# Optimization experiments

Hardware: AMD Instinct MI355X
Metric: run time of the kernel (lower is better)

Reference implementation:

```python
import jax, jax.numpy as jnp
import numpy as np

# Model dims (from module defaults / chosen plant dims)
B, T = 1024, 1024
NY, NX, NW, NU = 32, 16, 128, 8   # input(obs), state, nonlin, output(action)
DT = 0.01
N_ITER_COLD = 30   # torchdeq f_max_iter
N_ITER_WARM = 5    # solver_kwargs f_max_iter when reusing warm start
LOG_STD_INIT = -1.6094379124341003


def setup_inputs() -> dict:
    key = jax.random.key(0)
    ks = jax.random.split(key, 11)
    s = 0.1  # keep the implicit/recurrent dynamics stable over 1024 RK4 steps
    obs = jax.random.normal(ks[0], (B, T, NY), jnp.float32)
    x0 = jnp.zeros((B, NX), jnp.float32)
    A_T = (-0.5 * jnp.eye(NX) + 0.05 * jax.random.normal(ks[1], (NX, NX))).astype(jnp.float32)
    Bw_T = s * jax.random.normal(ks[2], (NW, NX), jnp.float32)
    By_T = s * jax.random.normal(ks[3], (NY, NX), jnp.float32)
    Cv_T = s * jax.random.normal(ks[4], (NX, NW), jnp.float32)
    Dvw_T = 0.05 * jax.random.normal(ks[5], (NW, NW), jnp.float32)  # small -> fixed-point contraction
    Dvy_T = s * jax.random.normal(ks[6], (NY, NW), jnp.float32)
    Cu_T = s * jax.random.normal(ks[7], (NX, NU), jnp.float32)
    Duw_T = s * jax.random.normal(ks[8], (NW, NU), jnp.float32)
    Duy_T = s * jax.random.normal(ks[9], (NY, NU), jnp.float32)
    log_stds = LOG_STD_INIT * jnp.ones((NU,), jnp.float32)
    return dict(obs=obs, x0=x0, A_T=A_T, Bw_T=Bw_T, By_T=By_T, Cv_T=Cv_T,
                Dvw_T=Dvw_T, Dvy_T=Dvy_T, Cu_T=Cu_T, Duw_T=Duw_T, Duy_T=Duy_T,
                log_stds=log_stds)


def reference(obs, x0, A_T, Bw_T, By_T, Cv_T, Dvw_T, Dvy_T, Cu_T, Duw_T, Duy_T, log_stds):
    def fp_solve(w0, bias, n_iter):
        # w = tanh(x@Cv_T + w@Dvw_T + y@Dvy_T); bias = x@Cv_T + y@Dvy_T precomputed
        def body(i, w):
            return jnp.tanh(bias + w @ Dvw_T)
        return jax.lax.fori_loop(0, n_iter, body, w0)

    def xdot(x, w, y):
        return x @ A_T + w @ Bw_T + y @ By_T

    def step(x, y, w_guess, n_w):
        y_bias = y @ Dvy_T  # [B, NW], reused across RK stages
        wk = fp_solve(w_guess, x @ Cv_T + y_bias, n_w)
        k1 = xdot(x, wk, y)
        def stage(xs, w_prev):
            ws = fp_solve(w_prev, xs @ Cv_T + y_bias, N_ITER_WARM)
            return xdot(xs, ws, y), ws
        k2, w2 = stage(x + 0.5 * DT * k1, wk)
        k3, w3 = stage(x + 0.5 * DT * k2, w2)
        k4, w4 = stage(x + DT * k3, w3)
        x_next = x + (DT / 6.0) * (k1 + 2.0 * k2 + 2.0 * k3 + k4)
        u = x @ Cu_T + wk @ Duw_T + y @ Duy_T  # action from current state/nonlin/obs
        return x_next, w4, u

    # First timestep: cold DEQ solve (30 iters), no warm start
    w0 = jnp.zeros((x0.shape[0], NW), x0.dtype)
    x1, wg, u0 = step(x0, obs[:, 0], w0, N_ITER_COLD)

    # Remaining timesteps: warm-started solves (5 iters), sequential via scan
    def scan_body(carry, y_t):
        x, wg = carry
        x_next, w_next, u = step(x, y_t, wg, N_ITER_WARM)
        return (x_next, w_next), u
    obs_rest = jnp.swapaxes(obs[:, 1:], 0, 1)  # [T-1, B, NY]
    _, us = jax.lax.scan(scan_body, (x1, wg), obs_rest)

    actions = jnp.concatenate([u0[:, None, :], jnp.swapaxes(us, 0, 1)], axis=1)  # [B, T, NU]
    outputs = jnp.concatenate(
        [actions, jnp.broadcast_to(log_stds, actions.shape)], axis=-1)  # [B, T, 2*NU]
    return outputs
```

## Files before the change

### kernel.cpp

```cpp
#include <hip/hip_runtime.h>
#include <hip/hip_bf16.h>


#define T_SZ 1024
#define NY 32
#define NX 16
#define NW 128
#define NU 8
#define DT_F 0.01f
#define NCOLD 30
#define NWARM 5
#define KAPPA 2.8853900817779268f

typedef __attribute__((ext_vector_type(8))) short bf8v;
typedef __attribute__((ext_vector_type(4))) float f4v;

#define MFMA16(a, b, c) __builtin_amdgcn_mfma_f32_16x16x32_bf16((a), (b), (c), 0, 0, 0)

__device__ __forceinline__ unsigned short f2bf(float f) {
  return __builtin_bit_cast(unsigned short, __float2bfloat16(f));
}
__device__ __forceinline__ float bf2f(unsigned short u) {
  return __bfloat162float(__builtin_bit_cast(__hip_bfloat16, u));
}
__device__ __forceinline__ short tanh_bf(float z) {
  float e = __builtin_amdgcn_exp2f(z);
  float r = __builtin_amdgcn_rcpf(e + 1.0f);
  return (short)f2bf(1.0f - 2.0f * r);
}

__global__ __launch_bounds__(256, 1) void rinn_kernel(
    const float* __restrict__ obs, const float* __restrict__ x0,
    const float* __restrict__ A_T, const float* __restrict__ Bw_T,
    const float* __restrict__ By_T, const float* __restrict__ Cv_T,
    const float* __restrict__ Dvw_T, const float* __restrict__ Dvy_T,
    const float* __restrict__ Cu_T, const float* __restrict__ Duw_T,
    const float* __restrict__ Duy_T, const float* __restrict__ log_stds,
    float* __restrict__ out) {
  __shared__ __align__(16) char wlds[8192];
  __shared__ __align__(16) char xlds[4096];

  const int tid = (int)threadIdx.x;
  const int wv = tid >> 6;
  const int lane = tid & 63;
  const int r = lane & 15;
  const int h = lane >> 4;
  const long grow = (long)(blockIdx.x * 16 + r);
  const int sw = (r & 7) << 4;
  const int rbase = r * 256;

  const int ro0 = (64 * wv + 16 * h) ^ sw;
  const int ro1 = (64 * ((wv + 1) & 3) + 16 * h) ^ sw;
  const int ro2 = (64 * ((wv + 2) & 3) + 16 * h) ^ sw;
  const int ro3 = (64 * ((wv + 3) & 3) + 16 * h) ^ sw;

  bf8v Adw[2][4], Acv[2], Ady[2];
#pragma unroll
  for (int gi = 0; gi < 2; ++gi) {
    const int j = 32 * wv + 8 * (r >> 2) + 4 * gi + (r & 3);
#pragma unroll
    for (int s = 0; s < 4; ++s) {
      const int f = (wv + s) & 3;
#pragma unroll
      for (int q = 0; q < 8; ++q)
        Adw[gi][s][q] = (short)f2bf(KAPPA * Dvw_T[(32 * f + 8 * h + q) * NW + j]);
    }
#pragma unroll
    for (int q = 0; q < 8; ++q) {
      Acv[gi][q] = (short)f2bf(KAPPA * Cv_T[((8 * h + q) & 15) * NW + j]);
      Ady[gi][q] = (short)f2bf(KAPPA * Dvy_T[(8 * h + q) * NW + j]);
    }
  }
  bf8v Ax, Akx[4], Ayx, Au, Aku[4], Ayu;
#pragma unroll
  for (int q = 0; q < 8; ++q) {
    int k = 8 * h + q;
    Ax[q] = (short)f2bf(A_T[(k & 15) * NX + r]);
    Ayx[q] = (short)f2bf(By_T[k * NX + r]);
    float cu = 0.f, dy = 0.f;
    if (wv == 1 && r < NU) { cu = Cu_T[(k & 15) * NU + r]; dy = Duy_T[k * NU + r]; }
    Au[q] = (short)f2bf(cu);
    Ayu[q] = (short)f2bf(dy);
  }
#pragma unroll
  for (int s = 0; s < 4; ++s) {
    const int f = (wv + s) & 3;
#pragma unroll
    for (int q = 0; q < 8; ++q) {
      int k = 32 * f + 8 * h + q;
      Akx[s][q] = (short)f2bf(Bw_T[k * NX + r]);
      float du = 0.f;
      if (wv == 1 && r < NU) du = Duw_T[k * NU + r];
      Aku[s][q] = (short)f2bf(du);
    }
  }
  f4v lsv;
#pragma unroll
  for (int i = 0; i < 4; ++i) lsv[i] = (h >= 2) ? log_stds[4 * (h - 2) + i] : 0.f;

  f4v xr;
#pragma unroll
  for (int i = 0; i < 4; ++i) xr[i] = x0[grow * NX + 4 * h + i];

  char* xbase = xlds + wv * 1024;
  auto write_x = [&](f4v v) {
    unsigned short b0 = f2bf(v[0]), b1 = f2bf(v[1]), b2 = f2bf(v[2]), b3 = f2bf(v[3]);
    uint2 hp, lp;
    hp.x = (unsigned)b0 | ((unsigned)b1 << 16);
    hp.y = (unsigned)b2 | ((unsigned)b3 << 16);
    lp.x = (unsigned)f2bf(v[0] - bf2f(b0)) | ((unsigned)f2bf(v[1] - bf2f(b1)) << 16);
    lp.y = (unsigned)f2bf(v[2] - bf2f(b2)) | ((unsigned)f2bf(v[3] - bf2f(b3)) << 16);
    *(uint2*)(xbase + r * 64 + 8 * h) = hp;
    *(uint2*)(xbase + r * 64 + 32 + 8 * h) = lp;
  };
  auto read_bx = [&]() { return *(const bf8v*)(xbase + r * 64 + 16 * h); };

  {
    uint4 z; z.x = z.y = z.z = z.w = 0u;
    ((uint4*)wlds)[tid] = z;
    write_x(xr);
  }
  __syncthreads();

  const float* orow = obs + grow * T_SZ * NY;
  bf8v By0, By1;
  {
    float yf[8];
#pragma unroll
    for (int q = 0; q < 8; ++q) yf[q] = orow[8 * h + q];
#pragma unroll
    for (int q = 0; q < 8; ++q) {
      unsigned short hi = f2bf(yf[q]);
      By0[q] = (short)hi;
      By1[q] = (short)f2bf(yf[q] - bf2f(hi));
    }
  }

  int co = 0;
  bf8v of8 = {};
  f4v cbias0, cbias1;

  auto solve_iter = [&]() {
    const char* wb = wlds + co;
    bf8v b1 = *(const bf8v*)(wb + rbase + ro1);
    bf8v b2 = *(const bf8v*)(wb + rbase + ro2);
    bf8v b3 = *(const bf8v*)(wb + rbase + ro3);
    f4v c0 = MFMA16(Adw[0][0], of8, cbias0);
    f4v c1 = MFMA16(Adw[1][0], of8, cbias1);
    c0 = MFMA16(Adw[0][1], b1, c0);  c1 = MFMA16(Adw[1][1], b1, c1);
    c0 = MFMA16(Adw[0][2], b2, c0);  c1 = MFMA16(Adw[1][2], b2, c1);
    c0 = MFMA16(Adw[0][3], b3, c0);  c1 = MFMA16(Adw[1][3], b3, c1);
    bf8v o;
    o[0] = tanh_bf(c0[0]); o[1] = tanh_bf(c0[1]); o[2] = tanh_bf(c0[2]); o[3] = tanh_bf(c0[3]);
    o[4] = tanh_bf(c1[0]); o[5] = tanh_bf(c1[1]); o[6] = tanh_bf(c1[2]); o[7] = tanh_bf(c1[3]);
    of8 = o;
    *(bf8v*)(wlds + (co ^ 4096) + rbase + ro0) = o;
    __syncthreads();
    co ^= 4096;
  };

  auto kchain = [&](bf8v bx, int t, bool do_u) -> f4v {
    const char* wb = wlds + co;
    bf8v b1 = *(const bf8v*)(wb + rbase + ro1);
    bf8v b2 = *(const bf8v*)(wb + rbase + ro2);
    bf8v b3 = *(const bf8v*)(wb + rbase + ro3);
    f4v z = {0.f, 0.f, 0.f, 0.f};
    f4v c = MFMA16(Ax, bx, z);
    c = MFMA16(Akx[0], of8, c);
    c = MFMA16(Akx[1], b1, c); c = MFMA16(Akx[2], b2, c); c = MFMA16(Akx[3], b3, c);
    c = MFMA16(Ayx, By0, c);   c = MFMA16(Ayx, By1, c);
    if (do_u && wv == 1) {
      f4v cu = MFMA16(Au, bx, z);
      cu = MFMA16(Aku[0], of8, cu);
      cu = MFMA16(Aku[1], b1, cu); cu = MFMA16(Aku[2], b2, cu); cu = MFMA16(Aku[3], b3, cu);
      cu = MFMA16(Ayu, By0, cu);   cu = MFMA16(Ayu, By1, cu);
      f4v sv;
#pragma unroll
      for (int i = 0; i < 4; ++i) sv[i] = (h < 2) ? cu[i] : lsv[i];
      *(f4v*)(out + (grow * T_SZ + t) * 16 + 4 * h) = sv;
    }
    return c;
  };

  for (int t = 0; t < T_SZ; ++t) {
    f4v zz = {0.f, 0.f, 0.f, 0.f};
    f4v cb0 = MFMA16(Ady[0], By0, zz); cb0 = MFMA16(Ady[0], By1, cb0);
    f4v cb1 = MFMA16(Ady[1], By0, zz); cb1 = MFMA16(Ady[1], By1, cb1);

    bf8v bx = read_bx();
    cbias0 = MFMA16(Acv[0], bx, cb0); cbias1 = MFMA16(Acv[1], bx, cb1);
    const int n1 = (t == 0) ? NCOLD : NWARM;
    for (int it = 0; it < n1; ++it) solve_iter();
    float yn[8];
    {
      const long tn = (t + 1 < T_SZ) ? (t + 1) : t;
#pragma unroll
      for (int q = 0; q < 8; ++q) yn[q] = orow[tn * NY + 8 * h + q];
    }
    f4v kv = kchain(bx, t, true);
    f4v acc = kv, xs;
#pragma unroll
    for (int i = 0; i < 4; ++i) xs[i] = xr[i] + (0.5f * DT_F) * kv[i];
    write_x(xs);

    bx = read_bx();
    cbias0 = MFMA16(Acv[0], bx, cb0); cbias1 = MFMA16(Acv[1], bx, cb1);
    for (int it = 0; it < NWARM; ++it) solve_iter();
    kv = kchain(bx, t, false);
#pragma unroll
    for (int i = 0; i < 4; ++i) { acc[i] += 2.f * kv[i]; xs[i] = xr[i] + (0.5f * DT_F) * kv[i]; }
    write_x(xs);

    bx = read_bx();
    cbias0 = MFMA16(Acv[0], bx, cb0); cbias1 = MFMA16(Acv[1], bx, cb1);
    for (int it = 0; it < NWARM; ++it) solve_iter();
    kv = kchain(bx, t, false);
#pragma unroll
    for (int i = 0; i < 4; ++i) { acc[i] += 2.f * kv[i]; xs[i] = xr[i] + DT_F * kv[i]; }
    write_x(xs);

    bx = read_bx();
    cbias0 = MFMA16(Acv[0], bx, cb0); cbias1 = MFMA16(Acv[1], bx, cb1);
    for (int it = 0; it < NWARM; ++it) solve_iter();
    kv = kchain(bx, t, false);
#pragma unroll
    for (int i = 0; i < 4; ++i) xr[i] += (DT_F / 6.f) * (acc[i] + kv[i]);
    write_x(xr);

#pragma unroll
    for (int q = 0; q < 8; ++q) {
      unsigned short hi = f2bf(yn[q]);
      By0[q] = (short)hi;
      By1[q] = (short)f2bf(yn[q] - bf2f(hi));
    }
  }
}

extern "C" void kernel_launch(void* const* d_in, const int* in_sizes, int n_in,
                              void* d_out, int out_size, void* d_ws, size_t ws_size,
                              hipStream_t stream) {
  (void)in_sizes; (void)n_in; (void)out_size; (void)d_ws; (void)ws_size;
  rinn_kernel<<<64, 256, 0, stream>>>(
      (const float*)d_in[0], (const float*)d_in[1], (const float*)d_in[2],
      (const float*)d_in[3], (const float*)d_in[4], (const float*)d_in[5],
      (const float*)d_in[6], (const float*)d_in[7], (const float*)d_in[8],
      (const float*)d_in[9], (const float*)d_in[10], (const float*)d_in[11],
      (float*)d_out);
}
```

Measured before the change: 6.200 ms.

## Fuse k-chain with next stage's first solve iteration and shuffle x via bpermute

Each RK stage's xdot computation is merged with the first fixed-point iteration of the following stage, so both share one set of LDS reads of w and one barrier. The x state is no longer passed through LDS; it is moved into MFMA fragment layout with ds_bpermute. __syncthreads is replaced by a custom barrier that waits only on LDS counters, which removes the per-stage barriers and LDS round-trips. The restructured loop must reproduce the original iteration counts, and the lighter barrier relies on only LDS traffic needing ordering.

```diff
diff --git a/kernel.cpp b/kernel.cpp
--- a/kernel.cpp
+++ b/kernel.cpp
@@ -28,6 +28,11 @@
   float r = __builtin_amdgcn_rcpf(e + 1.0f);
   return (short)f2bf(1.0f - 2.0f * r);
 }
+__device__ __forceinline__ void wave_barrier() {
+  asm volatile("s_waitcnt lgkmcnt(0)" ::: "memory");
+  __builtin_amdgcn_s_barrier();
+  asm volatile("" ::: "memory");
+}
 
 __global__ __launch_bounds__(256, 1) void rinn_kernel(
     const float* __restrict__ obs, const float* __restrict__ x0,
@@ -38,7 +43,6 @@
     const float* __restrict__ Duy_T, const float* __restrict__ log_stds,
     float* __restrict__ out) {
   __shared__ __align__(16) char wlds[8192];
-  __shared__ __align__(16) char xlds[4096];
 
   const int tid = (int)threadIdx.x;
   const int wv = tid >> 6;
@@ -54,6 +58,10 @@
   const int ro2 = (64 * ((wv + 2) & 3) + 16 * h) ^ sw;
   const int ro3 = (64 * ((wv + 3) & 3) + 16 * h) ^ sw;
 
+  const int ti0 = 4 * (r + 16 * ((2 * h) & 3));
+  const int ti1 = 4 * (r + 16 * ((2 * h + 1) & 3));
+  const bool hi_sel = (h < 2);
+
   bf8v Adw[2][4], Acv[2], Ady[2];
 #pragma unroll
   for (int gi = 0; gi < 2; ++gi) {
@@ -102,25 +110,10 @@
 #pragma unroll
   for (int i = 0; i < 4; ++i) xr[i] = x0[grow * NX + 4 * h + i];
 
-  char* xbase = xlds + wv * 1024;
-  auto write_x = [&](f4v v) {
-    unsigned short b0 = f2bf(v[0]), b1 = f2bf(v[1]), b2 = f2bf(v[2]), b3 = f2bf(v[3]);
-    uint2 hp, lp;
-    hp.x = (unsigned)b0 | ((unsigned)b1 << 16);
-    hp.y = (unsigned)b2 | ((unsigned)b3 << 16);
-    lp.x = (unsigned)f2bf(v[0] - bf2f(b0)) | ((unsigned)f2bf(v[1] - bf2f(b1)) << 16);
-    lp.y = (unsigned)f2bf(v[2] - bf2f(b2)) | ((unsigned)f2bf(v[3] - bf2f(b3)) << 16);
-    *(uint2*)(xbase + r * 64 + 8 * h) = hp;
-    *(uint2*)(xbase + r * 64 + 32 + 8 * h) = lp;
-  };
-  auto read_bx = [&]() { return *(const bf8v*)(xbase + r * 64 + 16 * h); };
-
   {
     uint4 z; z.x = z.y = z.z = z.w = 0u;
     ((uint4*)wlds)[tid] = z;
-    write_x(xr);
-  }
-  __syncthreads();
+  }
 
   const float* orow = obs + grow * T_SZ * NY;
   bf8v By0, By1;
@@ -135,10 +128,43 @@
       By1[q] = (short)f2bf(yf[q] - bf2f(hi));
     }
   }
+  wave_barrier();
+
+  auto x_to_bfrag = [&](f4v v) -> bf8v {
+    unsigned short hb0 = f2bf(v[0]), hb1 = f2bf(v[1]), hb2 = f2bf(v[2]), hb3 = f2bf(v[3]);
+    unsigned hiP0 = (unsigned)hb0 | ((unsigned)hb1 << 16);
+    unsigned hiP1 = (unsigned)hb2 | ((unsigned)hb3 << 16);
+    unsigned loP0 = (unsigned)f2bf(v[0] - bf2f(hb0)) | ((unsigned)f2bf(v[1] - bf2f(hb1)) << 16);
+    unsigned loP1 = (unsigned)f2bf(v[2] - bf2f(hb2)) | ((unsigned)f2bf(v[3] - bf2f(hb3)) << 16);
+    int a0 = __builtin_amdgcn_ds_bpermute(ti0, (int)hiP0);
+    int a1 = __builtin_amdgcn_ds_bpermute(ti0, (int)hiP1);
+    int a2 = __builtin_amdgcn_ds_bpermute(ti1, (int)hiP0);
+    int a3 = __builtin_amdgcn_ds_bpermute(ti1, (int)hiP1);
+    int b0 = __builtin_amdgcn_ds_bpermute(ti0, (int)loP0);
+    int b1_ = __builtin_amdgcn_ds_bpermute(ti0, (int)loP1);
+    int b2_ = __builtin_amdgcn_ds_bpermute(ti1, (int)loP0);
+    int b3_ = __builtin_amdgcn_ds_bpermute(ti1, (int)loP1);
+    int4 d;
+    d.x = hi_sel ? a0 : b0;
+    d.y = hi_sel ? a1 : b1_;
+    d.z = hi_sel ? a2 : b2_;
+    d.w = hi_sel ? a3 : b3_;
+    return __builtin_bit_cast(bf8v, d);
+  };
+
+  f4v cb0, cb1, cbias0, cbias1, acc;
+  bf8v bxc;
+  {
+    f4v z4 = {0.f, 0.f, 0.f, 0.f};
+    cb0 = MFMA16(Ady[0], By0, z4); cb0 = MFMA16(Ady[0], By1, cb0);
+    cb1 = MFMA16(Ady[1], By0, z4); cb1 = MFMA16(Ady[1], By1, cb1);
+    bxc = x_to_bfrag(xr);
+    cbias0 = MFMA16(Acv[0], bxc, cb0);
+    cbias1 = MFMA16(Acv[1], bxc, cb1);
+  }
 
   int co = 0;
   bf8v of8 = {};
-  f4v cbias0, cbias1;
 
   auto solve_iter = [&]() {
     const char* wb = wlds + co;
@@ -155,84 +181,94 @@
     o[4] = tanh_bf(c1[0]); o[5] = tanh_bf(c1[1]); o[6] = tanh_bf(c1[2]); o[7] = tanh_bf(c1[3]);
     of8 = o;
     *(bf8v*)(wlds + (co ^ 4096) + rbase + ro0) = o;
-    __syncthreads();
+    wave_barrier();
     co ^= 4096;
   };
 
-  auto kchain = [&](bf8v bx, int t, bool do_u) -> f4v {
+  for (int it = 0; it < NCOLD - 4; ++it) solve_iter();
+
+  float yn[8];
+
+  auto fusedB = [&](int mode, int t) {
     const char* wb = wlds + co;
     bf8v b1 = *(const bf8v*)(wb + rbase + ro1);
     bf8v b2 = *(const bf8v*)(wb + rbase + ro2);
     bf8v b3 = *(const bf8v*)(wb + rbase + ro3);
-    f4v z = {0.f, 0.f, 0.f, 0.f};
-    f4v c = MFMA16(Ax, bx, z);
-    c = MFMA16(Akx[0], of8, c);
-    c = MFMA16(Akx[1], b1, c); c = MFMA16(Akx[2], b2, c); c = MFMA16(Akx[3], b3, c);
-    c = MFMA16(Ayx, By0, c);   c = MFMA16(Ayx, By1, c);
-    if (do_u && wv == 1) {
-      f4v cu = MFMA16(Au, bx, z);
+    f4v z4 = {0.f, 0.f, 0.f, 0.f};
+    f4v kv = MFMA16(Ax, bxc, z4);
+    kv = MFMA16(Akx[0], of8, kv);
+    kv = MFMA16(Ayx, By0, kv);  kv = MFMA16(Ayx, By1, kv);
+    kv = MFMA16(Akx[1], b1, kv); kv = MFMA16(Akx[2], b2, kv); kv = MFMA16(Akx[3], b3, kv);
+    if (mode == 1 && wv == 1) {
+      f4v cu = MFMA16(Au, bxc, z4);
       cu = MFMA16(Aku[0], of8, cu);
+      cu = MFMA16(Ayu, By0, cu);  cu = MFMA16(Ayu, By1, cu);
       cu = MFMA16(Aku[1], b1, cu); cu = MFMA16(Aku[2], b2, cu); cu = MFMA16(Aku[3], b3, cu);
-      cu = MFMA16(Ayu, By0, cu);   cu = MFMA16(Ayu, By1, cu);
       f4v sv;
 #pragma unroll
       for (int i = 0; i < 4; ++i) sv[i] = (h < 2) ? cu[i] : lsv[i];
       *(f4v*)(out + (grow * T_SZ + t) * 16 + 4 * h) = sv;
     }
-    return c;
+    f4v xs;
+    if (mode == 1) {
+      acc = kv;
+#pragma unroll
+      for (int i = 0; i < 4; ++i) xs[i] = xr[i] + (0.5f * DT_F) * kv[i];
+    } else if (mode == 2) {
+#pragma unroll
+      for (int i = 0; i < 4; ++i) { acc[i] += 2.f * kv[i]; xs[i] = xr[i] + (0.5f * DT_F) * kv[i]; }
+    } else if (mode == 3) {
+#pragma unroll
+      for (int i = 0; i < 4; ++i) { acc[i] += 2.f * kv[i]; xs[i] = xr[i] + DT_F * kv[i]; }
+    } else {
+#pragma unroll
+      for (int i = 0; i < 4; ++i) xr[i] += (DT_F / 6.f) * (acc[i] + kv[i]);
+      xs = xr;
+    }
+    bf8v bxn = x_to_bfrag(xs);
+    if (mode == 4) {
+#pragma unroll
+      for (int q = 0; q < 8; ++q) {
+        unsigned short hi = f2bf(yn[q]);
+        By0[q] = (short)hi;
+        By1[q] = (short)f2bf(yn[q] - bf2f(hi));
+      }
+      cb0 = MFMA16(Ady[0], By0, z4); cb0 = MFMA16(Ady[0], By1, cb0);
+      cb1 = MFMA16(Ady[1], By0, z4); cb1 = MFMA16(Ady[1], By1, cb1);
+    }
+    cbias0 = MFMA16(Acv[0], bxn, cb0);
+    cbias1 = MFMA16(Acv[1], bxn, cb1);
+    f4v d0 = MFMA16(Adw[0][0], of8, z4);
+    d0 = MFMA16(Adw[0][1], b1, d0); d0 = MFMA16(Adw[0][2], b2, d0); d0 = MFMA16(Adw[0][3], b3, d0);
+    f4v d1 = MFMA16(Adw[1][0], of8, z4);
+    d1 = MFMA16(Adw[1][1], b1, d1); d1 = MFMA16(Adw[1][2], b2, d1); d1 = MFMA16(Adw[1][3], b3, d1);
+    f4v c0, c1;
+#pragma unroll
+    for (int i = 0; i < 4; ++i) { c0[i] = d0[i] + cbias0[i]; c1[i] = d1[i] + cbias1[i]; }
+    bf8v o;
+    o[0] = tanh_bf(c0[0]); o[1] = tanh_bf(c0[1]); o[2] = tanh_bf(c0[2]); o[3] = tanh_bf(c0[3]);
+    o[4] = tanh_bf(c1[0]); o[5] = tanh_bf(c1[1]); o[6] = tanh_bf(c1[2]); o[7] = tanh_bf(c1[3]);
+    of8 = o;
+    *(bf8v*)(wlds + (co ^ 4096) + rbase + ro0) = o;
+    wave_barrier();
+    co ^= 4096;
+    bxc = bxn;
   };
 
   for (int t = 0; t < T_SZ; ++t) {
-    f4v zz = {0.f, 0.f, 0.f, 0.f};
-    f4v cb0 = MFMA16(Ady[0], By0, zz); cb0 = MFMA16(Ady[0], By1, cb0);
-    f4v cb1 = MFMA16(Ady[1], By0, zz); cb1 = MFMA16(Ady[1], By1, cb1);
-
-    bf8v bx = read_bx();
-    cbias0 = MFMA16(Acv[0], bx, cb0); cbias1 = MFMA16(Acv[1], bx, cb1);
-    const int n1 = (t == 0) ? NCOLD : NWARM;
-    for (int it = 0; it < n1; ++it) solve_iter();
-    float yn[8];
+    for (int i = 0; i < 4; ++i) solve_iter();
+    fusedB(1, t);
     {
       const long tn = (t + 1 < T_SZ) ? (t + 1) : t;
 #pragma unroll
       for (int q = 0; q < 8; ++q) yn[q] = orow[tn * NY + 8 * h + q];
     }
-    f4v kv = kchain(bx, t, true);
-    f4v acc = kv, xs;
-#pragma unroll
-    for (int i = 0; i < 4; ++i) xs[i] = xr[i] + (0.5f * DT_F) * kv[i];
-    write_x(xs);
-
-    bx = read_bx();
-    cbias0 = MFMA16(Acv[0], bx, cb0); cbias1 = MFMA16(Acv[1], bx, cb1);
-    for (int it = 0; it < NWARM; ++it) solve_iter();
-    kv = kchain(bx, t, false);
-#pragma unroll
-    for (int i = 0; i < 4; ++i) { acc[i] += 2.f * kv[i]; xs[i] = xr[i] + (0.5f * DT_F) * kv[i]; }
-    write_x(xs);
-
-    bx = read_bx();
-    cbias0 = MFMA16(Acv[0], bx, cb0); cbias1 = MFMA16(Acv[1], bx, cb1);
-    for (int it = 0; it < NWARM; ++it) solve_iter();
-    kv = kchain(bx, t, false);
-#pragma unroll
-    for (int i = 0; i < 4; ++i) { acc[i] += 2.f * kv[i]; xs[i] = xr[i] + DT_F * kv[i]; }
-    write_x(xs);
-
-    bx = read_bx();
-    cbias0 = MFMA16(Acv[0], bx, cb0); cbias1 = MFMA16(Acv[1], bx, cb1);
-    for (int it = 0; it < NWARM; ++it) solve_iter();
-    kv = kchain(bx, t, false);
-#pragma unroll
-    for (int i = 0; i < 4; ++i) xr[i] += (DT_F / 6.f) * (acc[i] + kv[i]);
-    write_x(xr);
-
-#pragma unroll
-    for (int q = 0; q < 8; ++q) {
-      unsigned short hi = f2bf(yn[q]);
-      By0[q] = (short)hi;
-      By1[q] = (short)f2bf(yn[q] - bf2f(hi));
-    }
+    for (int i = 0; i < 4; ++i) solve_iter();
+    fusedB(2, t);
+    for (int i = 0; i < 4; ++i) solve_iter();
+    fusedB(3, t);
+    for (int i = 0; i < 4; ++i) solve_iter();
+    fusedB(4, t);
   }
 }
 
```

Result: no change. 6.213 ms (+0.2%).
